# Kernel tuning notes

Hardware: AMD Instinct MI355X
Metric: run time of the kernel (lower is better)

The kernel has to match this reference:

```python
import jax, jax.numpy as jnp
import numpy as np

B, S, D = 2, 1024, 512
NH, HD = 8, 64          # num_heads, head_dim
NS, F3 = 8, 1536        # shared experts, ffn_dim_shared = 3*D
E, F2 = 32, 1024        # routed experts, ffn_dim_routed = 2*D
R, K = 64, 4            # router_rank, num_activated_experts


def _ln(x, w, b, eps=1e-5):
    m = x.mean(-1, keepdims=True)
    v = ((x - m) ** 2).mean(-1, keepdims=True)
    return (x - m) * jax.lax.rsqrt(v + eps) * w + b


def _rms(x, w, eps=1e-6):
    return x * jax.lax.rsqrt((x * x).mean(-1, keepdims=True) + eps) * w


def _l2n(x, eps=1e-12):
    return x / jnp.maximum(jnp.linalg.norm(x, axis=-1, keepdims=True), eps)


def setup_inputs() -> dict:
    key = jax.random.key(0)
    ks = iter(jax.random.split(key, 40))
    sc = 0.02
    n = lambda shape: jax.random.normal(next(ks), shape, dtype=jnp.float32) * sc
    inp = {
        'x': jax.random.normal(next(ks), (B, S, D), dtype=jnp.float32),
        'ln1_w': jnp.ones((D,)), 'ln1_b': jnp.zeros((D,)),
        'ln2_w': jnp.ones((D,)), 'ln2_b': jnp.zeros((D,)),
        # per-head attention params, stacked over heads
        'q_w': n((NH, D, HD)), 'q_b': jnp.zeros((NH, HD)),
        'k_w': n((NH, D, HD)), 'k_b': jnp.zeros((NH, HD)),
        'v_w': n((NH, D, HD)), 'v_b': jnp.zeros((NH, HD)),
        'aw1': n((NH, D, HD // 2)), 'ab1': jnp.zeros((NH, HD // 2)),
        'aw2': n((NH, HD // 2, HD)), 'ab2': jnp.zeros((NH, HD)),
        'bw': n((NH, D, HD)), 'bb': jnp.zeros((NH, HD)),
        'scw1': n((NH, D, HD // 2)), 'scb1': jnp.zeros((NH, HD // 2)),
        'scw2': n((NH, HD // 2, HD)), 'scb2': jnp.zeros((NH, HD)),
        'arms_w': jnp.ones((NH, HD)),
        'l1_w': n((NH, HD, HD)), 'l1_b': jnp.zeros((NH, HD)),
        'out_w': n((D, D)), 'out_b': jnp.zeros((D,)),
        # MoE params
        'sh_rms': jnp.ones((NS, D)),
        'sh_w1': n((NS, D, F3)), 'sh_w2': n((NS, F3, D)), 'sh_w3': n((NS, D, F3)),
        'r_w1': n((E, D, F2)), 'r_w2': n((E, F2, D)), 'r_w3': n((E, D, F2)),
        'rd_w': n((D, R)), 'ru_w': n((R, E)),
    }
    return inp


def _forward(x, ln1_w, ln1_b, ln2_w, ln2_b, q_w, q_b, k_w, k_b, v_w, v_b,
             aw1, ab1, aw2, ab2, bw, bb, scw1, scb1, scw2, scb2, arms_w,
             l1_w, l1_b, out_w, out_b, sh_rms, sh_w1, sh_w2, sh_w3,
             r_w1, r_w2, r_w3, rd_w, ru_w):
    silu, sig = jax.nn.silu, jax.nn.sigmoid
    # ---- attention sublayer (dropout = identity in eval) ----
    residual = x
    xn = _ln(x, ln1_w, ln1_b)                                   # [B,S,D]
    q = _l2n(silu(jnp.einsum('bsd,hdk->bhsk', xn, q_w) + q_b[None, :, None, :]))
    k = _l2n(silu(jnp.einsum('bsd,hdk->bhsk', xn, k_w) + k_b[None, :, None, :]))
    v = silu(jnp.einsum('bsd,hdk->bhsk', xn, v_w) + v_b[None, :, None, :])
    alpha = sig(jnp.einsum('bhsr,hrk->bhsk',
                           jnp.einsum('bsd,hdr->bhsr', xn, aw1) + ab1[None, :, None, :],
                           aw2) + ab2[None, :, None, :])
    beta = sig(jnp.einsum('bsd,hdk->bhsk', xn, bw) + bb[None, :, None, :])
    shortcut = sig(jnp.einsum('bhsr,hrk->bhsk',
                              jnp.einsum('bsd,hdr->bhsr', xn, scw1) + scb1[None, :, None, :],
                              scw2) + scb2[None, :, None, :])
    v = v * alpha + beta
    scores = jnp.einsum('bhsk,bhtk->bhst', q, k) / jnp.sqrt(jnp.float32(HD))
    o = jnp.einsum('bhst,bhtk->bhsk', jax.nn.softmax(scores, axis=-1), v)
    o = _rms(o, arms_w[None, :, None, :]) * shortcut
    o = jnp.einsum('bhsk,hkj->bhsj', o, l1_w) + l1_b[None, :, None, :]
    o = o.transpose(0, 2, 1, 3).reshape(B, S, D)                # concat heads
    x = residual + (o @ out_w + out_b)
    # ---- MoE sublayer ----
    residual = x
    xf = _ln(x, ln2_w, ln2_b).reshape(-1, D)                    # [T,D]
    T = xf.shape[0]
    # shared experts (AdvancedExpert: rmsnorm -> swiglu -> +residual), averaged
    rb = xf * jax.lax.rsqrt((xf * xf).mean(-1, keepdims=True) + 1e-6)
    hn = rb[None] * sh_rms[:, None, :]                          # [NS,T,D]
    gate = silu(jnp.einsum('ntd,ndf->ntf', hn, sh_w1))
    val = jnp.einsum('ntd,ndf->ntf', hn, sh_w3)
    sh_out = jnp.einsum('ntf,nfd->ntd', gate * val, sh_w2) + xf[None]
    shared = sh_out.sum(0) / NS
    # router (low-rank) + top-k softmax weights
    logits = (xf @ rd_w) @ ru_w                                 # [T,E]
    top_v, top_i = jax.lax.top_k(logits, K)
    rw = jax.nn.softmax(top_v, axis=-1)                         # [T,K]
    w_full = jnp.zeros((T, E), xf.dtype).at[jnp.arange(T)[:, None], top_i].add(rw)
    # routed experts: dense compute, masked combine (same math)
    rg = silu(jnp.einsum('td,edf->etf', xf, r_w1))
    rv = jnp.einsum('td,edf->etf', xf, r_w3)
    eo = jnp.einsum('etf,efd->etd', rg * rv, r_w2)              # [E,T,D]
    routed = jnp.einsum('etd,te->td', eo, w_full)
    x = residual + (shared + routed).reshape(B, S, D)
    counts = jnp.zeros((E,), jnp.float32).at[top_i.reshape(-1)].add(1.0)
    load_balance_loss = jnp.var(counts, ddof=1)
    return x, load_balance_loss


def reference(x, ln1_w, ln1_b, ln2_w, ln2_b, q_w, q_b, k_w, k_b, v_w, v_b,
              aw1, ab1, aw2, ab2, bw, bb, scw1, scb1, scw2, scb2, arms_w,
              l1_w, l1_b, out_w, out_b, sh_rms, sh_w1, sh_w2, sh_w3,
              r_w1, r_w2, r_w3, rd_w, ru_w):
    return _forward(x, ln1_w, ln1_b, ln2_w, ln2_b, q_w, q_b, k_w, k_b, v_w, v_b,
                    aw1, ab1, aw2, ab2, bw, bb, scw1, scb1, scw2, scb2, arms_w,
                    l1_w, l1_b, out_w, out_b, sh_rms, sh_w1, sh_w2, sh_w3,
                    r_w1, r_w2, r_w3, rd_w, ru_w)
```

## Files before the change

kernel.cpp:

```cpp
#include <hip/hip_runtime.h>
#include <cmath>
#include <cstdint>


typedef __bf16 bf16;
typedef __bf16 bf16x8 __attribute__((ext_vector_type(8)));
typedef __bf16 bf16x4 __attribute__((ext_vector_type(4)));
typedef float  f32x4  __attribute__((ext_vector_type(4)));

static constexpr int Bb = 2, Ss = 1024, Dd = 512, NHh = 8, HDd = 64;
static constexpr int Tt = Bb * Ss;
static constexpr int NSs = 8, F3f = 1536;
static constexpr int Ee = 32, F2f = 1024;
static constexpr int SLOTCAP = 10240;
static constexpr int MAXTILE = 160;

__device__ inline float wavesum(float v) {
#pragma unroll
  for (int i = 1; i < 64; i <<= 1) v += __shfl_xor(v, i, 64);
  return v;
}
__device__ inline float blocksum(float v, float* sm) {
  v = wavesum(v);
  int wv = threadIdx.x >> 6;
  __syncthreads();
  if ((threadIdx.x & 63) == 0) sm[wv] = v;
  __syncthreads();
  return (sm[0] + sm[1]) + (sm[2] + sm[3]);
}
__device__ inline float silu_f(float x) { return x / (1.f + expf(-x)); }
__device__ inline float sigm_f(float x) { return 1.f / (1.f + expf(-x)); }

__device__ inline int is_f32(const unsigned short* __restrict__ xr) {
  int good = 0;
#pragma unroll
  for (int i = 0; i < 32; ++i) {
    unsigned e = (xr[2 * i] >> 7) & 0xFF;
    good += (e >= 110 && e <= 140);
  }
  return good < 16;
}

template <typename TB, int WANT, int ACT, int DUAL, int OUTBF, int ACCUM,
          int RESID, int ASCALE>
__global__ __launch_bounds__(256) void gemm_k(
    const unsigned short* __restrict__ xdet,
// ... 122 lines not shown
    sT[row][cc + 0] = v0; sT[row][cc + 1] = v1;
    sT[row][cc + 2] = v2; sT[row][cc + 3] = v3;
  }
  __syncthreads();
  bf16* Oz = Wt + (long)z * oBatch;
#pragma unroll
  for (int it = 0; it < 4; ++it) {
    int n = it * 16 + rr;
    bf16x4 ov;
#pragma unroll
    for (int j = 0; j < 4; ++j) ov[j] = (bf16)sT[cc + j][n];
    *(bf16x4*)(Oz + (long)(n0 + n) * K + k0 + cc) = ov;
  }
}

template <int DUAL, int ACCUM>
__global__ __launch_bounds__(256) void gemmT_k(
    const bf16* __restrict__ A, long aBatch, int lda,
    const bf16* __restrict__ B0t, const bf16* __restrict__ B1t, long bBatch,
    void* __restrict__ Cv, long cBatch, int ldc, int K, float scale) {
  __shared__ __align__(16) bf16 sA[128 * 40];
  __shared__ __align__(16) bf16 sB0[64 * 40];
  __shared__ __align__(16) bf16 sB1[DUAL ? 64 * 40 : 16];
  const int tid = threadIdx.x, wave = tid >> 6, lane = tid & 63;
  const int fm = lane & 15, quad = lane >> 4;
  const bf16* Az = A + (long)blockIdx.z * aBatch + (long)(blockIdx.x * 128) * lda;
  const bf16* B0z = B0t + (long)blockIdx.z * bBatch + (long)(blockIdx.y * 64) * K;
  const bf16* B1z = DUAL ? (B1t + (long)blockIdx.z * bBatch + (long)(blockIdx.y * 64) * K) : nullptr;
  f32x4 acc0[2][4], acc1[2][4];
  const f32x4 vz = {0.f, 0.f, 0.f, 0.f};
#pragma unroll
  for (int m = 0; m < 2; ++m)
#pragma unroll
    for (int n = 0; n < 4; ++n) { acc0[m][n] = vz; acc1[m][n] = vz; }
  const int srow = tid >> 2, sk0 = (tid & 3) * 8;
  const bf16* Ap0 = Az + (long)srow * lda + sk0;
  const bf16* Ap1 = Az + (long)(srow + 64) * lda + sk0;
  const bf16* Bp0 = B0z + (long)srow * K + sk0;
  const bf16* Bp1 = DUAL ? (B1z + (long)srow * K + sk0) : Bp0;
  bf16x8 rA0 = *(const bf16x8*)(Ap0);
  bf16x8 rA1 = *(const bf16x8*)(Ap1);
  bf16x8 rB0 = *(const bf16x8*)(Bp0);
  bf16x8 rB1 = rB0;
  if (DUAL) rB1 = *(const bf16x8*)(Bp1);
  for (int kb = 0; kb < K; kb += 32) {
    *(bf16x8*)(sA + srow * 40 + sk0) = rA0;
    *(bf16x8*)(sA + (srow + 64) * 40 + sk0) = rA1;
    *(bf16x8*)(sB0 + srow * 40 + sk0) = rB0;
    if (DUAL) *(bf16x8*)(sB1 + srow * 40 + sk0) = rB1;
    __syncthreads();
    int kn = kb + 32 < K ? kb + 32 : kb;
    rA0 = *(const bf16x8*)(Ap0 + kn);
    rA1 = *(const bf16x8*)(Ap1 + kn);
    rB0 = *(const bf16x8*)(Bp0 + kn);
    if (DUAL) rB1 = *(const bf16x8*)(Bp1 + kn);
    bf16x8 af0 = *(const bf16x8*)(sA + (wave * 32 + fm) * 40 + quad * 8);
    bf16x8 af1 = *(const bf16x8*)(sA + (wave * 32 + 16 + fm) * 40 + quad * 8);
#pragma unroll
    for (int nt = 0; nt < 4; ++nt) {
      bf16x8 b0 = *(const bf16x8*)(sB0 + (nt * 16 + fm) * 40 + quad * 8);
      acc0[0][nt] = __builtin_amdgcn_mfma_f32_16x16x32_bf16(af0, b0, acc0[0][nt], 0, 0, 0);
      acc0[1][nt] = __builtin_amdgcn_mfma_f32_16x16x32_bf16(af1, b0, acc0[1][nt], 0, 0, 0);
      if (DUAL) {
        bf16x8 b1 = *(const bf16x8*)(sB1 + (nt * 16 + fm) * 40 + quad * 8);
        acc1[0][nt] = __builtin_amdgcn_mfma_f32_16x16x32_bf16(af0, b1, acc1[0][nt], 0, 0, 0);
        acc1[1][nt] = __builtin_amdgcn_mfma_f32_16x16x32_bf16(af1, b1, acc1[1][nt], 0, 0, 0);
      }
    }
    __syncthreads();
  }
#pragma unroll
  for (int mt = 0; mt < 2; ++mt)
#pragma unroll
    for (int nt = 0; nt < 4; ++nt) {
      int col = blockIdx.y * 64 + nt * 16 + fm;
#pragma unroll
      for (int r = 0; r < 4; ++r) {
        int row = blockIdx.x * 128 + wave * 32 + mt * 16 + quad * 4 + r;
        long ci = (long)blockIdx.z * cBatch + (long)row * ldc + col;
        if (DUAL) {
          ((bf16*)Cv)[ci] = (bf16)(silu_f(acc0[mt][nt][r]) * acc1[mt][nt][r]);
        } else {
          float v = acc0[mt][nt][r] * scale;
          if (ACCUM == 1) atomicAdd((float*)Cv + ci, v);
          else if (ACCUM == 2) ((float*)Cv)[ci] = v;
          else ((bf16*)Cv)[ci] = (bf16)v;
        }
      }
    }
}

__global__ __launch_bounds__(256) void moeT1_k(
    const int* __restrict__ tileExp, const int* __restrict__ tileStart,
    const int* __restrict__ slotTok, const bf16* __restrict__ xfb,
    const bf16* __restrict__ W1t, const bf16* __restrict__ W3t,
    bf16* __restrict__ hid) {
  int e = tileExp[blockIdx.x];
  if (e < 0) return;
  int slot0 = tileStart[blockIdx.x];
  __shared__ int sTok[64];
  __shared__ __align__(16) bf16 sA[64 * 40];
  __shared__ __align__(16) bf16 sB0[128 * 40];
  __shared__ __align__(16) bf16 sB1[128 * 40];
  const int tid = threadIdx.x, wave = tid >> 6, lane = tid & 63;
  const int fm = lane & 15, quad = lane >> 4;
  const int wr = wave >> 1, wc = wave & 1;
  if (tid < 64) sTok[tid] = slotTok[slot0 + tid];
  __syncthreads();
  const bf16* B0 = W1t + (long)e * (F2f * 512) + (long)(blockIdx.y * 128) * 512;
  const bf16* B1 = W3t + (long)e * (F2f * 512) + (long)(blockIdx.y * 128) * 512;
  f32x4 acc0[2][4], acc1[2][4];
  const f32x4 vz = {0.f, 0.f, 0.f, 0.f};
#pragma unroll
  for (int m = 0; m < 2; ++m)
#pragma unroll
    for (int n = 0; n < 4; ++n) { acc0[m][n] = vz; acc1[m][n] = vz; }
  const int srow = tid >> 2, sk0 = (tid & 3) * 8;
  const bf16* Ap  = xfb + (long)sTok[srow] * 512 + sk0;
  const bf16* B0p = B0 + (long)srow * 512 + sk0;
  const bf16* B0q = B0 + (long)(srow + 64) * 512 + sk0;
  const bf16* B1p = B1 + (long)srow * 512 + sk0;
  const bf16* B1q = B1 + (long)(srow + 64) * 512 + sk0;
  bf16x8 rA  = *(const bf16x8*)(Ap);
  bf16x8 rB0 = *(const bf16x8*)(B0p);
  bf16x8 rB1 = *(const bf16x8*)(B0q);
  bf16x8 rB2 = *(const bf16x8*)(B1p);
  bf16x8 rB3 = *(const bf16x8*)(B1q);
  for (int kb = 0; kb < 512; kb += 32) {
    *(bf16x8*)(sA + srow * 40 + sk0) = rA;
    *(bf16x8*)(sB0 + srow * 40 + sk0) = rB0;
    *(bf16x8*)(sB0 + (srow + 64) * 40 + sk0) = rB1;
    *(bf16x8*)(sB1 + srow * 40 + sk0) = rB2;
    *(bf16x8*)(sB1 + (srow + 64) * 40 + sk0) = rB3;
    __syncthreads();
    int kn = kb + 32 < 512 ? kb + 32 : kb;
    rA  = *(const bf16x8*)(Ap + kn);
    rB0 = *(const bf16x8*)(B0p + kn);
    rB1 = *(const bf16x8*)(B0q + kn);
    rB2 = *(const bf16x8*)(B1p + kn);
    rB3 = *(const bf16x8*)(B1q + kn);
    bf16x8 af0 = *(const bf16x8*)(sA + (wr * 32 + fm) * 40 + quad * 8);
    bf16x8 af1 = *(const bf16x8*)(sA + (wr * 32 + 16 + fm) * 40 + quad * 8);
#pragma unroll
    for (int nt = 0; nt < 4; ++nt) {
      bf16x8 b0 = *(const bf16x8*)(sB0 + (wc * 64 + nt * 16 + fm) * 40 + quad * 8);
      acc0[0][nt] = __builtin_amdgcn_mfma_f32_16x16x32_bf16(af0, b0, acc0[0][nt], 0, 0, 0);
      acc0[1][nt] = __builtin_amdgcn_mfma_f32_16x16x32_bf16(af1, b0, acc0[1][nt], 0, 0, 0);
      bf16x8 b1 = *(const bf16x8*)(sB1 + (wc * 64 + nt * 16 + fm) * 40 + quad * 8);
      acc1[0][nt] = __builtin_amdgcn_mfma_f32_16x16x32_bf16(af0, b1, acc1[0][nt], 0, 0, 0);
      acc1[1][nt] = __builtin_amdgcn_mfma_f32_16x16x32_bf16(af1, b1, acc1[1][nt], 0, 0, 0);
    }
    __syncthreads();
  }
#pragma unroll
  for (int mt = 0; mt < 2; ++mt)
#pragma unroll
    for (int nt = 0; nt < 4; ++nt) {
      int col = blockIdx.y * 128 + wc * 64 + nt * 16 + fm;
#pragma unroll
      for (int r = 0; r < 4; ++r) {
        int row = wr * 32 + mt * 16 + quad * 4 + r;
        hid[(long)(slot0 + row) * F2f + col] =
            (bf16)(silu_f(acc0[mt][nt][r]) * acc1[mt][nt][r]);
      }
    }
}

template <int GATHER>
__global__ __launch_bounds__(256) void moeT2_k(
    const int* __restrict__ tileExp, const int* __restrict__ tileStart,
    const int* __restrict__ slotTok, const float* __restrict__ slotW,
    const bf16* __restrict__ hid, const bf16* __restrict__ W2t,
    float* __restrict__ acc, float* __restrict__ eoRt) {
  int e = tileExp[blockIdx.x];
  if (e < 0) return;
  int slot0 = tileStart[blockIdx.x];
  __shared__ int sTok[64];
  __shared__ float sW[64];
  __shared__ __align__(16) bf16 sA[64 * 40];
  __shared__ __align__(16) bf16 sB[128 * 40];
  const int tid = threadIdx.x, wave = tid >> 6, lane = tid & 63;
  const int fm = lane & 15, quad = lane >> 4;
  const int wr = wave >> 1, wc = wave & 1;
  if (tid < 64) { sTok[tid] = slotTok[slot0 + tid]; sW[tid] = slotW[slot0 + tid]; }
  const bf16* B = W2t + (long)e * (512 * F2f) + (long)(blockIdx.y * 128) * F2f;
  f32x4 acc0[2][4];
  const f32x4 vz = {0.f, 0.f, 0.f, 0.f};
#pragma unroll
  for (int m = 0; m < 2; ++m)
#pragma unroll
    for (int n = 0; n < 4; ++n) acc0[m][n] = vz;
  const int srow = tid >> 2, sk0 = (tid & 3) * 8;
  const bf16* Ap  = hid + (long)(slot0 + srow) * F2f + sk0;
  const bf16* Bp0 = B + (long)srow * F2f + sk0;
  const bf16* Bp1 = B + (long)(srow + 64) * F2f + sk0;
  bf16x8 rA  = *(const bf16x8*)(Ap);
  bf16x8 rB0 = *(const bf16x8*)(Bp0);
  bf16x8 rB1 = *(const bf16x8*)(Bp1);
  for (int kb = 0; kb < F2f; kb += 32) {
    *(bf16x8*)(sA + srow * 40 + sk0) = rA;
    *(bf16x8*)(sB + srow * 40 + sk0) = rB0;
    *(bf16x8*)(sB + (srow + 64) * 40 + sk0) = rB1;
    __syncthreads();
    int kn = kb + 32 < F2f ? kb + 32 : kb;
    rA  = *(const bf16x8*)(Ap + kn);
    rB0 = *(const bf16x8*)(Bp0 + kn);
    rB1 = *(const bf16x8*)(Bp1 + kn);
    bf16x8 af0 = *(const bf16x8*)(sA + (wr * 32 + fm) * 40 + quad * 8);
    bf16x8 af1 = *(const bf16x8*)(sA + (wr * 32 + 16 + fm) * 40 + quad * 8);
#pragma unroll
    for (int nt = 0; nt < 4; ++nt) {
      bf16x8 b0 = *(const bf16x8*)(sB + (wc * 64 + nt * 16 + fm) * 40 + quad * 8);
      acc0[0][nt] = __builtin_amdgcn_mfma_f32_16x16x32_bf16(af0, b0, acc0[0][nt], 0, 0, 0);
      acc0[1][nt] = __builtin_amdgcn_mfma_f32_16x16x32_bf16(af1, b0, acc0[1][nt], 0, 0, 0);
    }
    __syncthreads();
  }
#pragma unroll
  for (int mt = 0; mt < 2; ++mt)
#pragma unroll
    for (int nt = 0; nt < 4; ++nt) {
      int col = blockIdx.y * 128 + wc * 64 + nt * 16 + fm;
#pragma unroll
      for (int r = 0; r < 4; ++r) {
        int row = wr * 32 + mt * 16 + quad * 4 + r;
        if (GATHER) {
          eoRt[(long)(slot0 + row) * 512 + col] = acc0[mt][nt][r] * sW[row];
// ... 254 lines not shown
  for (int nt = 0; nt < 4; ++nt) {
    int col = nt * 16 + fm;
#pragma unroll
    for (int r = 0; r < 4; ++r) {
      int row = qrow0 + quad * 4 + r;
      O[base + (long)row * 64 + col] = (bf16)(oacc[nt][r] / l_run[r]);
    }
  }
}

template <typename TX, typename TW, int WANT>
__global__ __launch_bounds__(256) void ln_k(const unsigned short* __restrict__ xdet,
                                            const TX* __restrict__ xi,
                                            const TW* __restrict__ w,
                                            const TW* __restrict__ b,
                                            bf16* __restrict__ obf, float eps) {
  if (is_f32(xdet) != WANT) return;
  __shared__ float sm[4];
  long base = (long)blockIdx.x * 512;
  int tid = threadIdx.x;
  float x0 = (float)xi[base + tid], x1 = (float)xi[base + 256 + tid];
  float mean = blocksum(x0 + x1, sm) * (1.f / 512.f);
  float d0 = x0 - mean, d1 = x1 - mean;
  float var = blocksum(d0 * d0 + d1 * d1, sm) * (1.f / 512.f);
  float r = rsqrtf(var + eps);
  obf[base + tid] = (bf16)(d0 * r * (float)w[tid] + (float)b[tid]);
  obf[base + 256 + tid] = (bf16)(d1 * r * (float)w[256 + tid] + (float)b[256 + tid]);
}

__global__ __launch_bounds__(256) void rms_k(const bf16* __restrict__ xi,
                                             bf16* __restrict__ ob) {
  __shared__ float sm[4];
  long base = (long)blockIdx.x * 512;
  int tid = threadIdx.x;
  float x0 = (float)xi[base + tid], x1 = (float)xi[base + 256 + tid];
  float ms = blocksum(x0 * x0 + x1 * x1, sm) * (1.f / 512.f);
// ... 265 lines not shown
  const void* rw1  = d_in[30];
  const void* rw2  = d_in[31];
  const void* rw3  = d_in[32];
  const void* rdw  = d_in[33];
  const void* ruw  = d_in[34];
  const unsigned short* xdet = (const unsigned short*)x;

  constexpr size_t MB = 1u << 20;
  char* base = (char*)d_ws;
  bf16* xn    = (bf16*)(base + 0 * MB);
  bf16* qh    = (bf16*)(base + 2 * MB);
  bf16* kh    = (bf16*)(base + 4 * MB);
  bf16* vh    = (bf16*)(base + 6 * MB);
  bf16* beta  = (bf16*)(base + 8 * MB);
  bf16* ah    = (bf16*)(base + 10 * MB);
  bf16* alpha = (bf16*)(base + 12 * MB);
  bf16* sch   = (bf16*)(base + 8 * MB);
  bf16* shct  = (bf16*)(base + 14 * MB);
  bf16* oatt  = (bf16*)(base + 8 * MB);
  bf16* conc  = (bf16*)(base + 2 * MB);
  float* x2   = (float*)(base + 4 * MB);
  bf16* xfb   = (bf16*)(base + 0 * MB);
  bf16* rbb   = (bf16*)(base + 2 * MB);
  float* acc  = (float*)(base + 12 * MB);
  int*   hcnt = (int*)(base + 8 * MB);
  int*   hcur = hcnt + 32;
  int*   hseg = hcnt + 64;
  int*   hte  = hcnt + 96;
  int*   hts  = hcnt + 288;
  int*   heidx= hcnt + 512;
  float* hew  = (float*)(hcnt + 512 + 8192);
  int*   hstok= hcnt + 512 + 16384;
  float* hsw  = (float*)(hcnt + 512 + 16384 + 10240);
  int*   hslot= hcnt + 512 + 16384 + 20480;

  size_t rem = ws_size > (size_t)16 * MB ? ws_size - (size_t)16 * MB : 0;
  const size_t SH1B  = (size_t)NSs * F3f * Dd * 2;
  const size_t R1B   = (size_t)Ee * F2f * Dd * 2;
  const size_t HIDRT = (size_t)SLOTCAP * F2f * 2;
  const size_t HID1  = (size_t)Tt * F3f * 2;
  const size_t EORT  = (size_t)SLOTCAP * 512 * 4;
  const size_t EOSH  = (size_t)NSs * Tt * 512 * 4;
  const bool cvtRt = rem >= 3 * SH1B + 3 * R1B + HIDRT;
  const bool cvtSh = cvtRt || rem >= 3 * SH1B + HID1;
  char* cur = base + (size_t)16 * MB;
  bf16 *sh1t = nullptr, *sh3t = nullptr, *sh2t = nullptr;
  bf16 *r1t = nullptr, *r3t = nullptr, *r2t = nullptr;
  size_t used = 0;
  if (cvtSh) {
    sh1t = (bf16*)cur; cur += SH1B;
    sh3t = (bf16*)cur; cur += SH1B;
    sh2t = (bf16*)cur; cur += SH1B;
    used += 3 * SH1B;
  }
  if (cvtRt) {
    r1t = (bf16*)cur; cur += R1B;
    r3t = (bf16*)cur; cur += R1B;
    r2t = (bf16*)cur; cur += R1B;
    used += 3 * R1B;
  }
  bool gather = false;
  float* eoRt = nullptr;
  float* eoSh = nullptr;
  if (cvtRt && rem - used >= EORT + HIDRT) {
    eoRt = (float*)cur; cur += EORT; used += EORT; gather = true;
  }
  if (gather && rem - used >= EOSH + HIDRT) {
    eoSh = (float*)cur; cur += EOSH; used += EOSH;
  }
  bf16* hid; long hidElems;
  if (ws_size >= 20 * MB) {
    hid = (bf16*)cur;
    hidElems = (long)((base + ws_size) - cur) / 2;
  } else {
    hid = (bf16*)(base + 8 * MB + 256 * 1024);
    hidElems = (long)(4 * MB - 256 * 1024) / 2;
  }
  const bool accUsed = (eoSh == nullptr) || !gather;

  ln_k<float, float, 1><<<Tt, 256, 0, stream>>>(xdet, (const float*)x, (const float*)ln1w, (const float*)ln1b, xn, 1e-5f);
  ln_k<bf16, bf16, 0><<<Tt, 256, 0, stream>>>(xdet, (const bf16*)x, (const bf16*)ln1w, (const bf16*)ln1b, xn, 1e-5f);

  G<1,0,1,0,0,0>(dim3(32,1,8), stream, xdet, xn,0,512, nullptr,0,0, q_w,0,nullptr,0,(long)512*64,64, q_b,64, qh,(long)Tt*64,64, nullptr,0, 64,512,1.f);
  G<1,0,1,0,0,0>(dim3(32,1,8), stream, xdet, xn,0,512, nullptr,0,0, k_w,0,nullptr,0,(long)512*64,64, k_b,64, kh,(long)Tt*64,64, nullptr,0, 64,512,1.f);
  G<1,0,1,0,0,0>(dim3(32,1,8), stream, xdet, xn,0,512, nullptr,0,0, v_w,0,nullptr,0,(long)512*64,64, v_b,64, vh,(long)Tt*64,64, nullptr,0, 64,512,1.f);
  G<2,0,1,0,0,0>(dim3(32,1,8), stream, xdet, xn,0,512, nullptr,0,0, bw,0,nullptr,0,(long)512*64,64, bbv,64, beta,(long)Tt*64,64, nullptr,0, 64,512,1.f);
  G<0,0,1,0,0,0>(dim3(32,1,8), stream, xdet, xn,0,512, nullptr,0,0, aw1,0,nullptr,0,(long)512*32,32, ab1,32, ah,(long)Tt*32,32, nullptr,0, 32,512,1.f);
  G<2,0,1,0,0,0>(dim3(32,1,8), stream, xdet, ah,(long)Tt*32,32, nullptr,0,0, aw2,0,nullptr,0,(long)32*64,64, ab2,64, alpha,(long)Tt*64,64, nullptr,0, 64,32,1.f);

  postproj_k<<<NHh * Tt / 4, 256, 0, stream>>>(qh, kh, vh, alpha, beta);

  G<0,0,1,0,0,0>(dim3(32,1,8), stream, xdet, xn,0,512, nullptr,0,0, scw1,0,nullptr,0,(long)512*32,32, scb1,32, sch,(long)Tt*32,32, nullptr,0, 32,512,1.f);
  G<2,0,1,0,0,0>(dim3(32,1,8), stream, xdet, sch,(long)Tt*32,32, nullptr,0,0, scw2,0,nullptr,0,(long)32*64,64, scb2,64, shct,(long)Tt*64,64, nullptr,0, 64,32,1.f);

  attn_k<<<dim3(16, 16), 256, 0, stream>>>(qh, kh, vh, oatt);

  orms_k<float, 1><<<NHh * Tt / 4, 256, 0, stream>>>(xdet, oatt, (const float*)arms, shct);
  orms_k<bf16, 0><<<NHh * Tt / 4, 256, 0, stream>>>(xdet, oatt, (const bf16*)arms, shct);

  G<0,0,1,0,0,0>(dim3(32,1,8), stream, xdet, oatt,(long)Tt*64,64, nullptr,0,0, l1w,0,nullptr,0,(long)64*64,64, l1b,64, conc,64,512, nullptr,0, 64,64,1.f);
  G<0,0,0,0,1,0>(dim3(32,8,1), stream, xdet, conc,0,512, nullptr,0,0, outw,0,nullptr,0,0,512, outb,0, x2,0,512, x,512, 512,512,1.f);

  ln_k<float, float, 1><<<Tt, 256, 0, stream>>>(xdet, x2, (const float*)ln2w, (const float*)ln2b, xfb, 1e-5f);
  ln_k<float, bf16, 0><<<Tt, 256, 0, stream>>>(xdet, x2, (const bf16*)ln2w, (const bf16*)ln2b, xfb, 1e-5f);
  rms_k<<<Tt, 256, 0, stream>>>(xfb, rbb);
  if (accUsed) zero_k<<<256, 256, 0, stream>>>(acc, (long)Tt * 512);
  zero_k<<<1, 64, 0, stream>>>((float*)hcnt, 64);
  router_k<float, 1><<<Tt / 4, 256, 0, stream>>>(xdet, x2, (const float*)ln2w, (const float*)ln2b, (const float*)rdw, (const float*)ruw, heidx, hew, hcnt);
  router_k<bf16, 0><<<Tt / 4, 256, 0, stream>>>(xdet, x2, (const bf16*)ln2w, (const bf16*)ln2b, (const bf16*)rdw, (const bf16*)ruw, heidx, hew, hcnt);
  offsets_k<<<1, 64, 0, stream>>>(hcnt, hseg, hte, hts);
  scatter_k<<<Tt / 256, 256, 0, stream>>>(heidx, hew, hseg, hcur, hstok, hsw, hslot);
  pad_k<<<Ee, 64, 0, stream>>>(hcnt, hseg, hstok, hsw);

  if (cvtSh) {
    CVT<1>(stream, xdet, shw1, shrms, sh1t, 512, F3f, NSs, (long)512*F3f, 512, (long)F3f*512);
    CVT<1>(stream, xdet, shw3, shrms, sh3t, 512, F3f, NSs, (long)512*F3f, 512, (long)F3f*512);
    CVT<0>(stream, xdet, shw2, nullptr, sh2t, F3f, 512, NSs, (long)F3f*512, 0, (long)512*F3f);
  }
  if (cvtRt) {
    CVT<0>(stream, xdet, rw1, nullptr, r1t, 512, F2f, Ee, (long)512*F2f, 0, (long)F2f*512);
    CVT<0>(stream, xdet, rw3, nullptr, r3t, 512, F2f, Ee, (long)512*F2f, 0, (long)F2f*512);
    CVT<0>(stream, xdet, rw2, nullptr, r2t, F2f, 512, Ee, (long)F2f*512, 0, (long)512*F2f);
  }

  if (cvtSh) {
    int zB = (int)(((size_t)hidElems * 2) / HID1);
    if (zB > NSs) zB = NSs;
    if (zB < 1) zB = 1;
    for (int e0 = 0; e0 < NSs; e0 += zB) {
      int zc = NSs - e0 < zB ? NSs - e0 : zB;
      gemmT_k<1, 0><<<dim3(Tt / 128, F3f / 64, zc), 256, 0, stream>>>(
          rbb, 0, 512, sh1t + (long)e0 * F3f * 512, sh3t + (long)e0 * F3f * 512,
          (long)F3f * 512, hid, (long)Tt * F3f, F3f, 512, 1.f);
      if (eoSh) {
        gemmT_k<0, 2><<<dim3(Tt / 128, 512 / 64, zc), 256, 0, stream>>>(
            hid, (long)Tt * F3f, F3f, sh2t + (long)e0 * 512 * F3f, nullptr,
            (long)512 * F3f, eoSh + (long)e0 * Tt * 512, (long)Tt * 512, 512,
            F3f, 0.125f);
      } else {
        gemmT_k<0, 1><<<dim3(Tt / 128, 512 / 64, zc), 256, 0, stream>>>(
            hid, (long)Tt * F3f, F3f, sh2t + (long)e0 * 512 * F3f, nullptr,
            (long)512 * F3f, acc, 0, 512, F3f, 0.125f);
      }
    }
  } else {
    int PsS, zBsh;
    if (hidElems >= (long)Tt * F3f) {
      PsS = F3f;
      zBsh = (int)(hidElems / ((long)Tt * F3f)); if (zBsh > NSs) zBsh = NSs;
    } else {
      PsS = (int)((hidElems / Tt / 32) * 32); if (PsS > F3f) PsS = F3f;
      zBsh = 1;
    }
    for (int n0e = 0; n0e < NSs; n0e += zBsh) {
      int zc = NSs - n0e < zBsh ? NSs - n0e : zBsh;
      for (int off = 0; off < F3f; off += PsS) {
        int Np = F3f - off < PsS ? F3f - off : PsS;
// ... 43 lines not shown
```

Baseline: 999.3 us.

## Use direct global-to-LDS loads in GEMMs and fuse attention projections

Replaces the register-staged, padded-LDS loading in gemmT_k and the MoE tile kernels with global_load_lds direct loads into unpadded 32-wide LDS tiles, dropping the register prefetch. It also adds a weight-conversion kernel that transposes q/k/v/beta, alpha/shortcut and out-projection weights to bf16, so the per-head projections can run as one fused GEMM with bias and per-column activation, writing head-major output. The out-projection then fuses bias and residual from an fp32 copy of x saved by the first layernorm. Tradeoffs: the loads are no longer software-pipelined against compute, the unpadded LDS layout may cause bank conflicts, and the path needs extra workspace.

```diff
diff --git a/kernel.cpp b/kernel.cpp
--- a/kernel.cpp
+++ b/kernel.cpp
@@ -30,6 +30,12 @@
 }
 __device__ inline float silu_f(float x) { return x / (1.f + expf(-x)); }
 __device__ inline float sigm_f(float x) { return 1.f / (1.f + expf(-x)); }
+
+__device__ inline void gl16(const void* g, void* l) {
+  __builtin_amdgcn_global_load_lds(
+      (const __attribute__((address_space(1))) void*)g,
+      (__attribute__((address_space(3))) void*)l, 16, 0, 0);
+}
 
 __device__ inline int is_f32(const unsigned short* __restrict__ xr) {
   int good = 0;
@@ -182,55 +188,125 @@
   }
 }
 
-template <int DUAL, int ACCUM>
+template <typename TI, int WANT>
+__global__ __launch_bounds__(256) void atconv_k(
+    const unsigned short* __restrict__ xdet,
+    const TI* __restrict__ qw, const TI* __restrict__ kw,
+    const TI* __restrict__ vw, const TI* __restrict__ bw,
+    const TI* __restrict__ a1w, const TI* __restrict__ s1w,
+    const TI* __restrict__ ow,
+    const TI* __restrict__ qb, const TI* __restrict__ kb,
+    const TI* __restrict__ vb, const TI* __restrict__ bb,
+    const TI* __restrict__ a1b, const TI* __restrict__ s1b,
+    const TI* __restrict__ ob,
+    bf16* __restrict__ wqkvbT, bf16* __restrict__ wascT,
+    bf16* __restrict__ woutT, float* __restrict__ biasP) {
+  if (is_f32(xdet) != WANT) return;
+  const int tid = threadIdx.x;
+  const int b = blockIdx.x;
+  if (b == 448) {
+    for (int i = tid; i < 3072; i += 256) {
+      float v;
+      if (i < 512) v = (float)qb[i];
+      else if (i < 1024) v = (float)kb[i - 512];
+      else if (i < 1536) v = (float)vb[i - 1024];
+      else if (i < 2048) v = (float)bb[i - 1536];
+      else if (i < 2304) v = (float)a1b[i - 2048];
+      else if (i < 2560) v = (float)s1b[i - 2304];
+      else v = (float)ob[i - 2560];
+      biasP[i] = v;
+    }
+    return;
+  }
+  __shared__ float sT[64][65];
+  const TI* W; bf16* O; int ldw, N, k0, n0;
+  if (b < 256) {
+    int t = b >> 6, i = b & 63, h = i >> 3;
+    k0 = (i & 7) * 64; n0 = 0; ldw = 64; N = 64;
+    const TI* s = t == 0 ? qw : t == 1 ? kw : t == 2 ? vw : bw;
+    W = s + (long)h * 512 * 64;
+    O = wqkvbT + ((long)t * 512 + h * 64) * 512;
+  } else if (b < 384) {
+    int t = (b - 256) >> 6, i = (b - 256) & 63, h = i >> 3;
+    k0 = (i & 7) * 64; n0 = 0; ldw = 32; N = 32;
+    W = (t == 0 ? a1w : s1w) + (long)h * 512 * 32;
+    O = wascT + ((long)t * 256 + h * 32) * 512;
+  } else {
+    int i = b - 384;
+    k0 = (i >> 3) * 64; n0 = (i & 7) * 64; ldw = 512; N = 512;
+    W = ow; O = woutT;
+  }
+  const int rr = tid >> 4, cc = (tid & 15) * 4;
+#pragma unroll
+  for (int it = 0; it < 4; ++it) {
+    int row = it * 16 + rr;
+    float v0 = 0.f, v1 = 0.f, v2 = 0.f, v3 = 0.f;
+    if (n0 + cc < N) {
+      const TI* p = W + (long)(k0 + row) * ldw + n0 + cc;
+      v0 = (float)p[0]; v1 = (float)p[1]; v2 = (float)p[2]; v3 = (float)p[3];
+    }
+    sT[row][cc + 0] = v0; sT[row][cc + 1] = v1;
+    sT[row][cc + 2] = v2; sT[row][cc + 3] = v3;
+  }
+  __syncthreads();
+#pragma unroll
+  for (int it = 0; it < 4; ++it) {
+    int n = it * 16 + rr;
+    if (n0 + n < N) {
+      bf16x4 ov;
+#pragma unroll
+      for (int j = 0; j < 4; ++j) ov[j] = (bf16)sT[cc + j][n];
+      *(bf16x4*)(O + (long)(n0 + n) * 512 + k0 + cc) = ov;
+    }
+  }
+}
+
+template <int DUAL, int CMODE, int ACT, int HOUT>
 __global__ __launch_bounds__(256) void gemmT_k(
     const bf16* __restrict__ A, long aBatch, int lda,
     const bf16* __restrict__ B0t, const bf16* __restrict__ B1t, long bBatch,
-    void* __restrict__ Cv, long cBatch, int ldc, int K, float scale) {
-  __shared__ __align__(16) bf16 sA[128 * 40];
-  __shared__ __align__(16) bf16 sB0[64 * 40];
-  __shared__ __align__(16) bf16 sB1[DUAL ? 64 * 40 : 16];
+    const float* __restrict__ bias,
+    void* __restrict__ Cv, long cBatch, int ldc,
+    const float* __restrict__ resid,
+    int K, float scale) {
+  __shared__ __align__(16) bf16 sA[128 * 32];
+  __shared__ __align__(16) bf16 sB0[64 * 32];
+  __shared__ __align__(16) bf16 sB1[DUAL ? 64 * 32 : 16];
   const int tid = threadIdx.x, wave = tid >> 6, lane = tid & 63;
   const int fm = lane & 15, quad = lane >> 4;
   const bf16* Az = A + (long)blockIdx.z * aBatch + (long)(blockIdx.x * 128) * lda;
   const bf16* B0z = B0t + (long)blockIdx.z * bBatch + (long)(blockIdx.y * 64) * K;
   const bf16* B1z = DUAL ? (B1t + (long)blockIdx.z * bBatch + (long)(blockIdx.y * 64) * K) : nullptr;
+  const int srow = lane >> 2, scol = (lane & 3) * 8;
+  const bf16* gA0 = Az + (long)(wave * 32 + srow) * lda + scol;
+  const bf16* gA1 = Az + (long)(wave * 32 + 16 + srow) * lda + scol;
+  const bf16* gB0 = B0z + (long)(wave * 16 + srow) * K + scol;
+  const bf16* gB1 = DUAL ? (B1z + (long)(wave * 16 + srow) * K + scol) : nullptr;
+  bf16* lA0 = sA + (wave * 32) * 32;
+  bf16* lA1 = sA + (wave * 32 + 16) * 32;
+  bf16* lB0 = sB0 + (wave * 16) * 32;
+  bf16* lB1 = DUAL ? (sB1 + (wave * 16) * 32) : nullptr;
   f32x4 acc0[2][4], acc1[2][4];
   const f32x4 vz = {0.f, 0.f, 0.f, 0.f};
 #pragma unroll
   for (int m = 0; m < 2; ++m)
 #pragma unroll
     for (int n = 0; n < 4; ++n) { acc0[m][n] = vz; acc1[m][n] = vz; }
-  const int srow = tid >> 2, sk0 = (tid & 3) * 8;
-  const bf16* Ap0 = Az + (long)srow * lda + sk0;
-  const bf16* Ap1 = Az + (long)(srow + 64) * lda + sk0;
-  const bf16* Bp0 = B0z + (long)srow * K + sk0;
-  const bf16* Bp1 = DUAL ? (B1z + (long)srow * K + sk0) : Bp0;
-  bf16x8 rA0 = *(const bf16x8*)(Ap0);
-  bf16x8 rA1 = *(const bf16x8*)(Ap1);
-  bf16x8 rB0 = *(const bf16x8*)(Bp0);
-  bf16x8 rB1 = rB0;
-  if (DUAL) rB1 = *(const bf16x8*)(Bp1);
   for (int kb = 0; kb < K; kb += 32) {
-    *(bf16x8*)(sA + srow * 40 + sk0) = rA0;
-    *(bf16x8*)(sA + (srow + 64) * 40 + sk0) = rA1;
-    *(bf16x8*)(sB0 + srow * 40 + sk0) = rB0;
-    if (DUAL) *(bf16x8*)(sB1 + srow * 40 + sk0) = rB1;
-    __syncthreads();
-    int kn = kb + 32 < K ? kb + 32 : kb;
-    rA0 = *(const bf16x8*)(Ap0 + kn);
-    rA1 = *(const bf16x8*)(Ap1 + kn);
-    rB0 = *(const bf16x8*)(Bp0 + kn);
-    if (DUAL) rB1 = *(const bf16x8*)(Bp1 + kn);
-    bf16x8 af0 = *(const bf16x8*)(sA + (wave * 32 + fm) * 40 + quad * 8);
-    bf16x8 af1 = *(const bf16x8*)(sA + (wave * 32 + 16 + fm) * 40 + quad * 8);
+    gl16(gA0 + kb, lA0);
+    gl16(gA1 + kb, lA1);
+    gl16(gB0 + kb, lB0);
+    if (DUAL) gl16(gB1 + kb, lB1);
+    __syncthreads();
+    bf16x8 af0 = *(const bf16x8*)(sA + (wave * 32 + fm) * 32 + quad * 8);
+    bf16x8 af1 = *(const bf16x8*)(sA + (wave * 32 + 16 + fm) * 32 + quad * 8);
 #pragma unroll
     for (int nt = 0; nt < 4; ++nt) {
-      bf16x8 b0 = *(const bf16x8*)(sB0 + (nt * 16 + fm) * 40 + quad * 8);
+      bf16x8 b0 = *(const bf16x8*)(sB0 + (nt * 16 + fm) * 32 + quad * 8);
       acc0[0][nt] = __builtin_amdgcn_mfma_f32_16x16x32_bf16(af0, b0, acc0[0][nt], 0, 0, 0);
       acc0[1][nt] = __builtin_amdgcn_mfma_f32_16x16x32_bf16(af1, b0, acc0[1][nt], 0, 0, 0);
       if (DUAL) {
-        bf16x8 b1 = *(const bf16x8*)(sB1 + (nt * 16 + fm) * 40 + quad * 8);
+        bf16x8 b1 = *(const bf16x8*)(sB1 + (nt * 16 + fm) * 32 + quad * 8);
         acc1[0][nt] = __builtin_amdgcn_mfma_f32_16x16x32_bf16(af0, b1, acc1[0][nt], 0, 0, 0);
         acc1[1][nt] = __builtin_amdgcn_mfma_f32_16x16x32_bf16(af1, b1, acc1[1][nt], 0, 0, 0);
       }
@@ -245,13 +321,22 @@
 #pragma unroll
       for (int r = 0; r < 4; ++r) {
         int row = blockIdx.x * 128 + wave * 32 + mt * 16 + quad * 4 + r;
-        long ci = (long)blockIdx.z * cBatch + (long)row * ldc + col;
+        long ci;
+        if (HOUT)
+          ci = (((long)(col >> HOUT) * Tt + row) << HOUT) + (col & ((1 << HOUT) - 1));
+        else
+          ci = (long)blockIdx.z * cBatch + (long)row * ldc + col;
         if (DUAL) {
           ((bf16*)Cv)[ci] = (bf16)(silu_f(acc0[mt][nt][r]) * acc1[mt][nt][r]);
         } else {
           float v = acc0[mt][nt][r] * scale;
-          if (ACCUM == 1) atomicAdd((float*)Cv + ci, v);
-          else if (ACCUM == 2) ((float*)Cv)[ci] = v;
+          if (bias) v += bias[col];
+          if (ACT == 1) v = silu_f(v);
+          else if (ACT == 2) v = sigm_f(v);
+          else if (ACT == 3) v = (col < 1536) ? silu_f(v) : sigm_f(v);
+          if (CMODE == 1) atomicAdd((float*)Cv + ci, v);
+          else if (CMODE == 2) ((float*)Cv)[ci] = v;
+          else if (CMODE == 3) ((float*)Cv)[ci] = v + resid[(long)row * ldc + col];
           else ((bf16*)Cv)[ci] = (bf16)v;
         }
       }
@@ -267,54 +352,49 @@
   if (e < 0) return;
   int slot0 = tileStart[blockIdx.x];
   __shared__ int sTok[64];
-  __shared__ __align__(16) bf16 sA[64 * 40];
-  __shared__ __align__(16) bf16 sB0[128 * 40];
-  __shared__ __align__(16) bf16 sB1[128 * 40];
+  __shared__ __align__(16) bf16 sA[64 * 32];
+  __shared__ __align__(16) bf16 sB0[128 * 32];
+  __shared__ __align__(16) bf16 sB1[128 * 32];
   const int tid = threadIdx.x, wave = tid >> 6, lane = tid & 63;
   const int fm = lane & 15, quad = lane >> 4;
   const int wr = wave >> 1, wc = wave & 1;
   if (tid < 64) sTok[tid] = slotTok[slot0 + tid];
   __syncthreads();
+  const int srow = lane >> 2, scol = (lane & 3) * 8;
+  const int myTok = sTok[wave * 16 + srow];
+  const bf16* gA = xfb + (long)myTok * 512 + scol;
   const bf16* B0 = W1t + (long)e * (F2f * 512) + (long)(blockIdx.y * 128) * 512;
   const bf16* B1 = W3t + (long)e * (F2f * 512) + (long)(blockIdx.y * 128) * 512;
+  const bf16* gB00 = B0 + (long)(wave * 32 + srow) * 512 + scol;
+  const bf16* gB01 = B0 + (long)(wave * 32 + 16 + srow) * 512 + scol;
+  const bf16* gB10 = B1 + (long)(wave * 32 + srow) * 512 + scol;
+  const bf16* gB11 = B1 + (long)(wave * 32 + 16 + srow) * 512 + scol;
+  bf16* lA = sA + (wave * 16) * 32;
+  bf16* lB00 = sB0 + (wave * 32) * 32;
+  bf16* lB01 = sB0 + (wave * 32 + 16) * 32;
+  bf16* lB10 = sB1 + (wave * 32) * 32;
+  bf16* lB11 = sB1 + (wave * 32 + 16) * 32;
   f32x4 acc0[2][4], acc1[2][4];
   const f32x4 vz = {0.f, 0.f, 0.f, 0.f};
 #pragma unroll
   for (int m = 0; m < 2; ++m)
 #pragma unroll
     for (int n = 0; n < 4; ++n) { acc0[m][n] = vz; acc1[m][n] = vz; }
-  const int srow = tid >> 2, sk0 = (tid & 3) * 8;
-  const bf16* Ap  = xfb + (long)sTok[srow] * 512 + sk0;
-  const bf16* B0p = B0 + (long)srow * 512 + sk0;
-  const bf16* B0q = B0 + (long)(srow + 64) * 512 + sk0;
-  const bf16* B1p = B1 + (long)srow * 512 + sk0;
-  const bf16* B1q = B1 + (long)(srow + 64) * 512 + sk0;
-  bf16x8 rA  = *(const bf16x8*)(Ap);
-  bf16x8 rB0 = *(const bf16x8*)(B0p);
-  bf16x8 rB1 = *(const bf16x8*)(B0q);
-  bf16x8 rB2 = *(const bf16x8*)(B1p);
-  bf16x8 rB3 = *(const bf16x8*)(B1q);
   for (int kb = 0; kb < 512; kb += 32) {
-    *(bf16x8*)(sA + srow * 40 + sk0) = rA;
-    *(bf16x8*)(sB0 + srow * 40 + sk0) = rB0;
-    *(bf16x8*)(sB0 + (srow + 64) * 40 + sk0) = rB1;
-    *(bf16x8*)(sB1 + srow * 40 + sk0) = rB2;
-    *(bf16x8*)(sB1 + (srow + 64) * 40 + sk0) = rB3;
-    __syncthreads();
-    int kn = kb + 32 < 512 ? kb + 32 : kb;
-    rA  = *(const bf16x8*)(Ap + kn);
-    rB0 = *(const bf16x8*)(B0p + kn);
-    rB1 = *(const bf16x8*)(B0q + kn);
-    rB2 = *(const bf16x8*)(B1p + kn);
-    rB3 = *(const bf16x8*)(B1q + kn);
-    bf16x8 af0 = *(const bf16x8*)(sA + (wr * 32 + fm) * 40 + quad * 8);
-    bf16x8 af1 = *(const bf16x8*)(sA + (wr * 32 + 16 + fm) * 40 + quad * 8);
+    gl16(gA + kb, lA);
+    gl16(gB00 + kb, lB00);
+    gl16(gB01 + kb, lB01);
+    gl16(gB10 + kb, lB10);
+    gl16(gB11 + kb, lB11);
+    __syncthreads();
+    bf16x8 af0 = *(const bf16x8*)(sA + (wr * 32 + fm) * 32 + quad * 8);
+    bf16x8 af1 = *(const bf16x8*)(sA + (wr * 32 + 16 + fm) * 32 + quad * 8);
 #pragma unroll
     for (int nt = 0; nt < 4; ++nt) {
-      bf16x8 b0 = *(const bf16x8*)(sB0 + (wc * 64 + nt * 16 + fm) * 40 + quad * 8);
+      bf16x8 b0 = *(const bf16x8*)(sB0 + (wc * 64 + nt * 16 + fm) * 32 + quad * 8);
       acc0[0][nt] = __builtin_amdgcn_mfma_f32_16x16x32_bf16(af0, b0, acc0[0][nt], 0, 0, 0);
       acc0[1][nt] = __builtin_amdgcn_mfma_f32_16x16x32_bf16(af1, b0, acc0[1][nt], 0, 0, 0);
-      bf16x8 b1 = *(const bf16x8*)(sB1 + (wc * 64 + nt * 16 + fm) * 40 + quad * 8);
+      bf16x8 b1 = *(const bf16x8*)(sB1 + (wc * 64 + nt * 16 + fm) * 32 + quad * 8);
       acc1[0][nt] = __builtin_amdgcn_mfma_f32_16x16x32_bf16(af0, b1, acc1[0][nt], 0, 0, 0);
       acc1[1][nt] = __builtin_amdgcn_mfma_f32_16x16x32_bf16(af1, b1, acc1[1][nt], 0, 0, 0);
     }
@@ -345,40 +425,36 @@
   int slot0 = tileStart[blockIdx.x];
   __shared__ int sTok[64];
   __shared__ float sW[64];
-  __shared__ __align__(16) bf16 sA[64 * 40];
-  __shared__ __align__(16) bf16 sB[128 * 40];
+  __shared__ __align__(16) bf16 sA[64 * 32];
+  __shared__ __align__(16) bf16 sB[128 * 32];
   const int tid = threadIdx.x, wave = tid >> 6, lane = tid & 63;
   const int fm = lane & 15, quad = lane >> 4;
   const int wr = wave >> 1, wc = wave & 1;
   if (tid < 64) { sTok[tid] = slotTok[slot0 + tid]; sW[tid] = slotW[slot0 + tid]; }
+  const int srow = lane >> 2, scol = (lane & 3) * 8;
+  const bf16* gA = hid + (long)(slot0 + wave * 16 + srow) * F2f + scol;
   const bf16* B = W2t + (long)e * (512 * F2f) + (long)(blockIdx.y * 128) * F2f;
+  const bf16* gB0 = B + (long)(wave * 32 + srow) * F2f + scol;
+  const bf16* gB1 = B + (long)(wave * 32 + 16 + srow) * F2f + scol;
+  bf16* lA = sA + (wave * 16) * 32;
+  bf16* lB0 = sB + (wave * 32) * 32;
+  bf16* lB1 = sB + (wave * 32 + 16) * 32;
   f32x4 acc0[2][4];
   const f32x4 vz = {0.f, 0.f, 0.f, 0.f};
 #pragma unroll
   for (int m = 0; m < 2; ++m)
 #pragma unroll
     for (int n = 0; n < 4; ++n) acc0[m][n] = vz;
-  const int srow = tid >> 2, sk0 = (tid & 3) * 8;
-  const bf16* Ap  = hid + (long)(slot0 + srow) * F2f + sk0;
-  const bf16* Bp0 = B + (long)srow * F2f + sk0;
-  const bf16* Bp1 = B + (long)(srow + 64) * F2f + sk0;
-  bf16x8 rA  = *(const bf16x8*)(Ap);
-  bf16x8 rB0 = *(const bf16x8*)(Bp0);
-  bf16x8 rB1 = *(const bf16x8*)(Bp1);
   for (int kb = 0; kb < F2f; kb += 32) {
-    *(bf16x8*)(sA + srow * 40 + sk0) = rA;
-    *(bf16x8*)(sB + srow * 40 + sk0) = rB0;
-    *(bf16x8*)(sB + (srow + 64) * 40 + sk0) = rB1;
-    __syncthreads();
-    int kn = kb + 32 < F2f ? kb + 32 : kb;
-    rA  = *(const bf16x8*)(Ap + kn);
-    rB0 = *(const bf16x8*)(Bp0 + kn);
-    rB1 = *(const bf16x8*)(Bp1 + kn);
-    bf16x8 af0 = *(const bf16x8*)(sA + (wr * 32 + fm) * 40 + quad * 8);
-    bf16x8 af1 = *(const bf16x8*)(sA + (wr * 32 + 16 + fm) * 40 + quad * 8);
+    gl16(gA + kb, lA);
+    gl16(gB0 + kb, lB0);
+    gl16(gB1 + kb, lB1);
+    __syncthreads();
+    bf16x8 af0 = *(const bf16x8*)(sA + (wr * 32 + fm) * 32 + quad * 8);
+    bf16x8 af1 = *(const bf16x8*)(sA + (wr * 32 + 16 + fm) * 32 + quad * 8);
 #pragma unroll
     for (int nt = 0; nt < 4; ++nt) {
-      bf16x8 b0 = *(const bf16x8*)(sB + (wc * 64 + nt * 16 + fm) * 40 + quad * 8);
+      bf16x8 b0 = *(const bf16x8*)(sB + (wc * 64 + nt * 16 + fm) * 32 + quad * 8);
       acc0[0][nt] = __builtin_amdgcn_mfma_f32_16x16x32_bf16(af0, b0, acc0[0][nt], 0, 0, 0);
       acc0[1][nt] = __builtin_amdgcn_mfma_f32_16x16x32_bf16(af1, b0, acc0[1][nt], 0, 0, 0);
     }
@@ -663,12 +739,14 @@
                                             const TX* __restrict__ xi,
                                             const TW* __restrict__ w,
                                             const TW* __restrict__ b,
-                                            bf16* __restrict__ obf, float eps) {
+                                            bf16* __restrict__ obf,
+                                            float* __restrict__ xraw, float eps) {
   if (is_f32(xdet) != WANT) return;
   __shared__ float sm[4];
   long base = (long)blockIdx.x * 512;
   int tid = threadIdx.x;
   float x0 = (float)xi[base + tid], x1 = (float)xi[base + 256 + tid];
+  if (xraw) { xraw[base + tid] = x0; xraw[base + 256 + tid] = x1; }
   float mean = blocksum(x0 + x1, sm) * (1.f / 512.f);
   float d0 = x0 - mean, d1 = x1 - mean;
   float var = blocksum(d0 * d0 + d1 * d1, sm) * (1.f / 512.f);
@@ -964,6 +1042,8 @@
   bf16* vh    = (bf16*)(base + 6 * MB);
   bf16* beta  = (bf16*)(base + 8 * MB);
   bf16* ah    = (bf16*)(base + 10 * MB);
+  bf16* ah2   = (bf16*)(base + 10 * MB);
+  bf16* sch2  = (bf16*)(base + 10 * MB) + (long)Tt * 256;
   bf16* alpha = (bf16*)(base + 12 * MB);
   bf16* sch   = (bf16*)(base + 8 * MB);
   bf16* shct  = (bf16*)(base + 14 * MB);
@@ -991,6 +1071,12 @@
   const size_t HID1  = (size_t)Tt * F3f * 2;
   const size_t EORT  = (size_t)SLOTCAP * 512 * 4;
   const size_t EOSH  = (size_t)NSs * Tt * 512 * 4;
+  const size_t WQKVB = (size_t)4 * 512 * 512 * 2;
+  const size_t WASC  = (size_t)512 * 512 * 2;
+  const size_t WOUT  = (size_t)512 * 512 * 2;
+  const size_t BIASB = 4096 * 4;
+  const size_t XF32  = (size_t)Tt * 512 * 4;
+  const size_t ATTNB = WQKVB + WASC + WOUT + BIASB + XF32;
   const bool cvtRt = rem >= 3 * SH1B + 3 * R1B + HIDRT;
   const bool cvtSh = cvtRt || rem >= 3 * SH1B + HID1;
   char* cur = base + (size_t)16 * MB;
@@ -1009,6 +1095,18 @@
     r2t = (bf16*)cur; cur += R1B;
     used += 3 * R1B;
   }
+  const size_t minHid = cvtRt ? HIDRT : (cvtSh ? HID1 : 0);
+  bool cvtAttn = cvtSh && (rem - used >= ATTNB + minHid);
+  bf16 *wqkvbT = nullptr, *wascT = nullptr, *woutT = nullptr;
+  float *biasP = nullptr, *xf32 = nullptr;
+  if (cvtAttn) {
+    wqkvbT = (bf16*)cur; cur += WQKVB;
+    wascT  = (bf16*)cur; cur += WASC;
+    woutT  = (bf16*)cur; cur += WOUT;
+    biasP  = (float*)cur; cur += BIASB;
+    xf32   = (float*)cur; cur += XF32;
+    used += ATTNB;
+  }
   bool gather = false;
   float* eoRt = nullptr;
   float* eoSh = nullptr;
@@ -1028,20 +1126,51 @@
   }
   const bool accUsed = (eoSh == nullptr) || !gather;
 
-  ln_k<float, float, 1><<<Tt, 256, 0, stream>>>(xdet, (const float*)x, (const float*)ln1w, (const float*)ln1b, xn, 1e-5f);
-  ln_k<bf16, bf16, 0><<<Tt, 256, 0, stream>>>(xdet, (const bf16*)x, (const bf16*)ln1w, (const bf16*)ln1b, xn, 1e-5f);
-
-  G<1,0,1,0,0,0>(dim3(32,1,8), stream, xdet, xn,0,512, nullptr,0,0, q_w,0,nullptr,0,(long)512*64,64, q_b,64, qh,(long)Tt*64,64, nullptr,0, 64,512,1.f);
-  G<1,0,1,0,0,0>(dim3(32,1,8), stream, xdet, xn,0,512, nullptr,0,0, k_w,0,nullptr,0,(long)512*64,64, k_b,64, kh,(long)Tt*64,64, nullptr,0, 64,512,1.f);
-  G<1,0,1,0,0,0>(dim3(32,1,8), stream, xdet, xn,0,512, nullptr,0,0, v_w,0,nullptr,0,(long)512*64,64, v_b,64, vh,(long)Tt*64,64, nullptr,0, 64,512,1.f);
-  G<2,0,1,0,0,0>(dim3(32,1,8), stream, xdet, xn,0,512, nullptr,0,0, bw,0,nullptr,0,(long)512*64,64, bbv,64, beta,(long)Tt*64,64, nullptr,0, 64,512,1.f);
-  G<0,0,1,0,0,0>(dim3(32,1,8), stream, xdet, xn,0,512, nullptr,0,0, aw1,0,nullptr,0,(long)512*32,32, ab1,32, ah,(long)Tt*32,32, nullptr,0, 32,512,1.f);
-  G<2,0,1,0,0,0>(dim3(32,1,8), stream, xdet, ah,(long)Tt*32,32, nullptr,0,0, aw2,0,nullptr,0,(long)32*64,64, ab2,64, alpha,(long)Tt*64,64, nullptr,0, 64,32,1.f);
+  if (cvtAttn) {
+    atconv_k<float, 1><<<449, 256, 0, stream>>>(
+        xdet, (const float*)q_w, (const float*)k_w, (const float*)v_w, (const float*)bw,
+        (const float*)aw1, (const float*)scw1, (const float*)outw,
+        (const float*)q_b, (const float*)k_b, (const float*)v_b, (const float*)bbv,
+        (const float*)ab1, (const float*)scb1, (const float*)outb,
+        wqkvbT, wascT, woutT, biasP);
+    atconv_k<bf16, 0><<<449, 256, 0, stream>>>(
+        xdet, (const bf16*)q_w, (const bf16*)k_w, (const bf16*)v_w, (const bf16*)bw,
+        (const bf16*)aw1, (const bf16*)scw1, (const bf16*)outw,
+        (const bf16*)q_b, (const bf16*)k_b, (const bf16*)v_b, (const bf16*)bbv,
+        (const bf16*)ab1, (const bf16*)scb1, (const bf16*)outb,
+        wqkvbT, wascT, woutT, biasP);
+  }
+
+  ln_k<float, float, 1><<<Tt, 256, 0, stream>>>(xdet, (const float*)x, (const float*)ln1w, (const float*)ln1b, xn, cvtAttn ? xf32 : nullptr, 1e-5f);
+  ln_k<bf16, bf16, 0><<<Tt, 256, 0, stream>>>(xdet, (const bf16*)x, (const bf16*)ln1w, (const bf16*)ln1b, xn, cvtAttn ? xf32 : nullptr, 1e-5f);
+
+  if (cvtAttn) {
+    gemmT_k<0, 0, 3, 6><<<dim3(16, 32, 1), 256, 0, stream>>>(
+        xn, 0, 512, wqkvbT, nullptr, 0, biasP, qh, 0, 64, nullptr, 512, 1.f);
+    gemmT_k<0, 0, 0, 5><<<dim3(16, 8, 1), 256, 0, stream>>>(
+        xn, 0, 512, wascT, nullptr, 0, biasP + 2048, ah2, 0, 32, nullptr, 512, 1.f);
+  } else {
+    G<1,0,1,0,0,0>(dim3(32,1,8), stream, xdet, xn,0,512, nullptr,0,0, q_w,0,nullptr,0,(long)512*64,64, q_b,64, qh,(long)Tt*64,64, nullptr,0, 64,512,1.f);
+    G<1,0,1,0,0,0>(dim3(32,1,8), stream, xdet, xn,0,512, nullptr,0,0, k_w,0,nullptr,0,(long)512*64,64, k_b,64, kh,(long)Tt*64,64, nullptr,0, 64,512,1.f);
+    G<1,0,1,0,0,0>(dim3(32,1,8), stream, xdet, xn,0,512, nullptr,0,0, v_w,0,nullptr,0,(long)512*64,64, v_b,64, vh,(long)Tt*64,64, nullptr,0, 64,512,1.f);
+    G<2,0,1,0,0,0>(dim3(32,1,8), stream, xdet, xn,0,512, nullptr,0,0, bw,0,nullptr,0,(long)512*64,64, bbv,64, beta,(long)Tt*64,64, nullptr,0, 64,512,1.f);
+    G<0,0,1,0,0,0>(dim3(32,1,8), stream, xdet, xn,0,512, nullptr,0,0, aw1,0,nullptr,0,(long)512*32,32, ab1,32, ah,(long)Tt*32,32, nullptr,0, 32,512,1.f);
+  }
+
+  {
+    const bf16* ahA = cvtAttn ? ah2 : ah;
+    G<2,0,1,0,0,0>(dim3(32,1,8), stream, xdet, ahA,(long)Tt*32,32, nullptr,0,0, aw2,0,nullptr,0,(long)32*64,64, ab2,64, alpha,(long)Tt*64,64, nullptr,0, 64,32,1.f);
+  }
 
   postproj_k<<<NHh * Tt / 4, 256, 0, stream>>>(qh, kh, vh, alpha, beta);
 
-  G<0,0,1,0,0,0>(dim3(32,1,8), stream, xdet, xn,0,512, nullptr,0,0, scw1,0,nullptr,0,(long)512*32,32, scb1,32, sch,(long)Tt*32,32, nullptr,0, 32,512,1.f);
-  G<2,0,1,0,0,0>(dim3(32,1,8), stream, xdet, sch,(long)Tt*32,32, nullptr,0,0, scw2,0,nullptr,0,(long)32*64,64, scb2,64, shct,(long)Tt*64,64, nullptr,0, 64,32,1.f);
+  if (!cvtAttn) {
+    G<0,0,1,0,0,0>(dim3(32,1,8), stream, xdet, xn,0,512, nullptr,0,0, scw1,0,nullptr,0,(long)512*32,32, scb1,32, sch,(long)Tt*32,32, nullptr,0, 32,512,1.f);
+  }
+  {
+    const bf16* schA = cvtAttn ? sch2 : sch;
+    G<2,0,1,0,0,0>(dim3(32,1,8), stream, xdet, schA,(long)Tt*32,32, nullptr,0,0, scw2,0,nullptr,0,(long)32*64,64, scb2,64, shct,(long)Tt*64,64, nullptr,0, 64,32,1.f);
+  }
 
   attn_k<<<dim3(16, 16), 256, 0, stream>>>(qh, kh, vh, oatt);
 
@@ -1049,10 +1178,16 @@
   orms_k<bf16, 0><<<NHh * Tt / 4, 256, 0, stream>>>(xdet, oatt, (const bf16*)arms, shct);
 
   G<0,0,1,0,0,0>(dim3(32,1,8), stream, xdet, oatt,(long)Tt*64,64, nullptr,0,0, l1w,0,nullptr,0,(long)64*64,64, l1b,64, conc,64,512, nullptr,0, 64,64,1.f);
-  G<0,0,0,0,1,0>(dim3(32,8,1), stream, xdet, conc,0,512, nullptr,0,0, outw,0,nullptr,0,0,512, outb,0, x2,0,512, x,512, 512,512,1.f);
-
-  ln_k<float, float, 1><<<Tt, 256, 0, stream>>>(xdet, x2, (const float*)ln2w, (const float*)ln2b, xfb, 1e-5f);
-  ln_k<float, bf16, 0><<<Tt, 256, 0, stream>>>(xdet, x2, (const bf16*)ln2w, (const bf16*)ln2b, xfb, 1e-5f);
+
+  if (cvtAttn) {
+    gemmT_k<0, 3, 0, 0><<<dim3(16, 8, 1), 256, 0, stream>>>(
+        conc, 0, 512, woutT, nullptr, 0, biasP + 2560, x2, 0, 512, xf32, 512, 1.f);
+  } else {
+    G<0,0,0,0,1,0>(dim3(32,8,1), stream, xdet, conc,0,512, nullptr,0,0, outw,0,nullptr,0,0,512, outb,0, x2,0,512, x,512, 512,512,1.f);
+  }
+
+  ln_k<float, float, 1><<<Tt, 256, 0, stream>>>(xdet, x2, (const float*)ln2w, (const float*)ln2b, xfb, nullptr, 1e-5f);
+  ln_k<float, bf16, 0><<<Tt, 256, 0, stream>>>(xdet, x2, (const bf16*)ln2w, (const bf16*)ln2b, xfb, nullptr, 1e-5f);
   rms_k<<<Tt, 256, 0, stream>>>(xfb, rbb);
   if (accUsed) zero_k<<<256, 256, 0, stream>>>(acc, (long)Tt * 512);
   zero_k<<<1, 64, 0, stream>>>((float*)hcnt, 64);
@@ -1079,18 +1214,18 @@
     if (zB < 1) zB = 1;
     for (int e0 = 0; e0 < NSs; e0 += zB) {
       int zc = NSs - e0 < zB ? NSs - e0 : zB;
-      gemmT_k<1, 0><<<dim3(Tt / 128, F3f / 64, zc), 256, 0, stream>>>(
+      gemmT_k<1, 0, 0, 0><<<dim3(Tt / 128, F3f / 64, zc), 256, 0, stream>>>(
           rbb, 0, 512, sh1t + (long)e0 * F3f * 512, sh3t + (long)e0 * F3f * 512,
-          (long)F3f * 512, hid, (long)Tt * F3f, F3f, 512, 1.f);
+          (long)F3f * 512, nullptr, hid, (long)Tt * F3f, F3f, nullptr, 512, 1.f);
       if (eoSh) {
-        gemmT_k<0, 2><<<dim3(Tt / 128, 512 / 64, zc), 256, 0, stream>>>(
+        gemmT_k<0, 2, 0, 0><<<dim3(Tt / 128, 512 / 64, zc), 256, 0, stream>>>(
             hid, (long)Tt * F3f, F3f, sh2t + (long)e0 * 512 * F3f, nullptr,
-            (long)512 * F3f, eoSh + (long)e0 * Tt * 512, (long)Tt * 512, 512,
-            F3f, 0.125f);
+            (long)512 * F3f, nullptr, eoSh + (long)e0 * Tt * 512, (long)Tt * 512,
+            512, nullptr, F3f, 0.125f);
       } else {
-        gemmT_k<0, 1><<<dim3(Tt / 128, 512 / 64, zc), 256, 0, stream>>>(
+        gemmT_k<0, 1, 0, 0><<<dim3(Tt / 128, 512 / 64, zc), 256, 0, stream>>>(
             hid, (long)Tt * F3f, F3f, sh2t + (long)e0 * 512 * F3f, nullptr,
-            (long)512 * F3f, acc, 0, 512, F3f, 0.125f);
+            (long)512 * F3f, nullptr, acc, 0, 512, nullptr, F3f, 0.125f);
       }
     }
   } else {
```

Measured after the change: 895.9 us. -10.3%, faster.
